# Kernel optimization log

Hardware: AMD Instinct MI355X
Metric: run time of the kernel (lower is better)

Reference implementation:

```python
import jax, jax.numpy as jnp
import numpy as np

TAIL_BOUND = 3.0
MIN_BIN_WIDTH = 1e-3
MIN_BIN_HEIGHT = 1e-3
SEARCH_EPS = 1e-6


def setup_inputs() -> dict:
    key = jax.random.key(0)
    k1, k2, k3, k4, k5 = jax.random.split(key, 5)
    B, D, K = 8192, 256, 8
    return {
        "x": jax.random.normal(k1, (B, D), dtype=jnp.float32),
        "w_": jax.random.normal(k2, (B, D, K), dtype=jnp.float32),
        "h_": jax.random.normal(k3, (B, D, K), dtype=jnp.float32),
        "dl_": jax.random.normal(k4, (B, D, 1), dtype=jnp.float32),
        "dr_": jax.random.normal(k5, (B, D, 1), dtype=jnp.float32),
    }


def _cumknots(unnorm, min_bin):
    # softmax -> min-width floor -> cumsum with exact 0/1 endpoints
    num_bins = unnorm.shape[-1]
    w = jax.nn.softmax(unnorm, axis=-1)
    w = min_bin + (1.0 - min_bin * num_bins) * w
    cum = jnp.cumsum(w, axis=-1)
    cum = cum.at[..., -1].set(1.0)
    pad = [(0, 0)] * (cum.ndim - 1) + [(1, 0)]
    cum = jnp.pad(cum, pad)
    return w, cum


def reference(x, w_, h_, dl_, dr_):
    num_bins = w_.shape[-1]
    left = bottom = -TAIL_BOUND
    right = top = TAIL_BOUND

    inside = (x >= left) & (x <= right)

    # map to unit interval; clamp keeps masked-out lanes numerically safe
    t = jnp.clip((x - left) / (right - left), 0.0, 1.0)

    widths, cumwidths = _cumknots(w_, MIN_BIN_WIDTH)       # [B,D,K], [B,D,K+1]
    heights, cumheights = _cumknots(h_, MIN_BIN_HEIGHT)

    slopes = heights / widths                              # [B,D,K]
    min1 = jnp.minimum(jnp.abs(slopes[..., :-1]), jnp.abs(slopes[..., 1:]))
    min2 = 0.5 * (widths[..., 1:] * slopes[..., :-1] + widths[..., :-1] * slopes[..., 1:]) \
           / (widths[..., :-1] + widths[..., 1:])
    mins = jnp.minimum(min1, min2)                         # [B,D,K-1]

    d_left = jax.nn.sigmoid(dl_) * 3.0 * slopes[..., :1]
    d_right = jax.nn.sigmoid(dr_) * 3.0 * slopes[..., -1:]
    d_mid = mins * (jnp.sign(slopes[..., :-1]) + jnp.sign(slopes[..., 1:]))
    derivs = jnp.concatenate([d_left, d_mid, d_right], axis=-1)  # [B,D,K+1]

    a = (derivs[..., :-1] + derivs[..., 1:] - 2.0 * slopes) / widths ** 2
    b = (3.0 * slopes - 2.0 * derivs[..., :-1] - derivs[..., 1:]) / widths
    c = derivs[..., :-1]
    d = cumheights[..., :-1]

    # searchsorted: sum(t >= knots) - 1, with eps bump on the last knot
    knots = cumwidths.at[..., -1].add(SEARCH_EPS)
    bin_idx = jnp.sum((t[..., None] >= knots).astype(jnp.int32), axis=-1) - 1
    bin_idx = jnp.clip(bin_idx, 0, num_bins - 1)[..., None]  # [B,D,1]

    take = lambda arr: jnp.take_along_axis(arr, bin_idx, axis=-1)[..., 0]
    ia, ib, ic, id_ = take(a), take(b), take(c), take(d)
    lw = take(cumwidths)

    sx = t - lw
    out_s = ia * sx ** 3 + ib * sx ** 2 + ic * sx + id_
    lad_s = jnp.log(jnp.abs(3.0 * ia * sx ** 2 + 2.0 * ib * sx + ic))

    out_s = jnp.clip(out_s, 0.0, 1.0) * (top - bottom) + bottom
    lad_s = lad_s + jnp.log(top - bottom) - jnp.log(right - left)

    outputs = jnp.where(inside, out_s, x)          # identity tails
    logabsdet = jnp.where(inside, lad_s, 0.0)
    return outputs, logabsdet
```

## Files before the change

kernel.cpp:

```cpp
#include <hip/hip_runtime.h>
#include <math.h>


constexpr int K = 8;
constexpr float TAIL = 3.0f;
constexpr float MIN_BIN = 0.001f;
constexpr float SEARCH_EPS = 1e-6f;

__device__ __forceinline__ float rcpf(float v) {
    return __builtin_amdgcn_rcpf(v);
}

__device__ __forceinline__ float signf(float v) {
    return (v > 0.0f ? 1.0f : (v < 0.0f ? -1.0f : 0.0f));
}

__global__ __launch_bounds__(256) void cbs_kernel(
    const float* __restrict__ x_,
    const float* __restrict__ w_,
    const float* __restrict__ h_,
    const float* __restrict__ dl_,
    const float* __restrict__ dr_,
    float* __restrict__ out,
    float* __restrict__ lad,
    int n)
{
    int i = blockIdx.x * blockDim.x + threadIdx.x;
    if (i >= n) return;

    const float4* w4 = (const float4*)w_ + 2 * (size_t)i;
    const float4* h4 = (const float4*)h_ + 2 * (size_t)i;
    float4 wa = w4[0], wb = w4[1];
    float4 ha = h4[0], hb = h4[1];

    float wr[K] = {wa.x, wa.y, wa.z, wa.w, wb.x, wb.y, wb.z, wb.w};
    float hr[K] = {ha.x, ha.y, ha.z, ha.w, hb.x, hb.y, hb.z, hb.w};

    float xv  = x_[i];
    float dlv = dl_[i];
    float drv = dr_[i];

    float mw = wr[0];
    #pragma unroll
    for (int k = 1; k < K; k++) mw = fmaxf(mw, wr[k]);
    float sw = 0.0f;
    #pragma unroll
    for (int k = 0; k < K; k++) { wr[k] = __expf(wr[k] - mw); sw += wr[k]; }
    float inv_sw = rcpf(sw);
    #pragma unroll
    for (int k = 0; k < K; k++) wr[k] = MIN_BIN + (1.0f - MIN_BIN * K) * (wr[k] * inv_sw);

    float mh = hr[0];
    #pragma unroll
    for (int k = 1; k < K; k++) mh = fmaxf(mh, hr[k]);
    float sh = 0.0f;
    #pragma unroll
    for (int k = 0; k < K; k++) { hr[k] = __expf(hr[k] - mh); sh += hr[k]; }
    float inv_sh = rcpf(sh);
    #pragma unroll
    for (int k = 0; k < K; k++) hr[k] = MIN_BIN + (1.0f - MIN_BIN * K) * (hr[k] * inv_sh);

    float cw[K + 1]; cw[0] = 0.0f;
    #pragma unroll
    for (int k = 0; k < K; k++) cw[k + 1] = cw[k] + wr[k];
    float ch[K + 1]; ch[0] = 0.0f;
    #pragma unroll
    for (int k = 0; k < K; k++) ch[k + 1] = ch[k] + hr[k];

    float s[K];
    #pragma unroll
    for (int k = 0; k < K; k++) s[k] = hr[k] * rcpf(wr[k]);

    float dv[K + 1];
    dv[0] = rcpf(1.0f + __expf(-dlv)) * 3.0f * s[0];
    dv[K] = rcpf(1.0f + __expf(-drv)) * 3.0f * s[K - 1];
    #pragma unroll
    for (int k = 0; k < K - 1; k++) {
        float m1 = fminf(fabsf(s[k]), fabsf(s[k + 1]));
        float m2 = 0.5f * (wr[k + 1] * s[k] + wr[k] * s[k + 1]) * rcpf(wr[k] + wr[k + 1]);
        float mn = fminf(m1, m2);
        dv[k + 1] = mn * (signf(s[k]) + signf(s[k + 1]));
    }

    float t = (xv + TAIL) * (1.0f / (2.0f * TAIL));
    t = fminf(fmaxf(t, 0.0f), 1.0f);

    int bin = 0;
    #pragma unroll
    for (int j = 1; j < K; j++) bin += (t >= cw[j]) ? 1 : 0;
    bin += (t >= 1.0f + SEARCH_EPS) ? 1 : 0;
    if (bin > K - 1) bin = K - 1;

    float wk = wr[0], sk = s[0], d0 = dv[0], d1 = dv[1], lw = cw[0], dd = ch[0];
    #pragma unroll
    for (int k = 1; k < K; k++) {
        bool sel = (bin == k);
        wk = sel ? wr[k]     : wk;
        sk = sel ? s[k]      : sk;
        d0 = sel ? dv[k]     : d0;
        d1 = sel ? dv[k + 1] : d1;
        lw = sel ? cw[k]     : lw;
        dd = sel ? ch[k]     : dd;
    }

    float inv_wk = rcpf(wk);
    float ia = (d0 + d1 - 2.0f * sk) * inv_wk * inv_wk;
    float ib = (3.0f * sk - 2.0f * d0 - d1) * inv_wk;
    float ic = d0;

    float sx = t - lw;
    float out_s = ((ia * sx + ib) * sx + ic) * sx + dd;
    float der   = (3.0f * ia * sx + 2.0f * ib) * sx + ic;
    float lad_s = __logf(fabsf(der));

    out_s = fminf(fmaxf(out_s, 0.0f), 1.0f) * (2.0f * TAIL) - TAIL;

    bool inside = (xv >= -TAIL) && (xv <= TAIL);
    out[i] = inside ? out_s : xv;
    lad[i] = inside ? lad_s : 0.0f;
}

extern "C" void kernel_launch(void* const* d_in, const int* in_sizes, int n_in,
                              void* d_out, int out_size, void* d_ws, size_t ws_size,
                              hipStream_t stream) {
    const float* x  = (const float*)d_in[0];
    const float* w  = (const float*)d_in[1];
    const float* h  = (const float*)d_in[2];
    const float* dl = (const float*)d_in[3];
    const float* dr = (const float*)d_in[4];
    int n = in_sizes[0];
    float* out = (float*)d_out;
    float* lad = out + n;

    const int threads = 256;
    const int blocks = (n + threads - 1) / threads;
    cbs_kernel<<<blocks, threads, 0, stream>>>(x, w, h, dl, dr, out, lad, n);
}
```

Baseline: 174.9 us.

## Process four elements per thread with vectorized IO and simplified spline math

Each thread now handles four consecutive elements, using float4 loads for x, dl and dr and float4 stores for both outputs. The softmax drops the max subtraction, the derivative formula is rewritten algebraically with fewer ops and no sign branches, and the bin search is folded into the predicated select loop. Launch bounds now request higher occupancy. The changes cut instruction count and memory transactions per element, but exp without the max shift can overflow for large logits, and the base>=n guard assumes n is a multiple of four.

New measurement: 179.0 us. +2.3%, slower.

```diff
diff --git a/kernel.cpp b/kernel.cpp
--- a/kernel.cpp
+++ b/kernel.cpp
@@ -3,19 +3,15 @@
 
 
 constexpr int K = 8;
+constexpr int E = 4;
 constexpr float TAIL = 3.0f;
 constexpr float MIN_BIN = 0.001f;
-constexpr float SEARCH_EPS = 1e-6f;
 
 __device__ __forceinline__ float rcpf(float v) {
     return __builtin_amdgcn_rcpf(v);
 }
 
-__device__ __forceinline__ float signf(float v) {
-    return (v > 0.0f ? 1.0f : (v < 0.0f ? -1.0f : 0.0f));
-}
-
-__global__ __launch_bounds__(256) void cbs_kernel(
+__global__ __launch_bounds__(256, 4) void cbs_kernel(
     const float* __restrict__ x_,
     const float* __restrict__ w_,
     const float* __restrict__ h_,
@@ -25,99 +21,102 @@
     float* __restrict__ lad,
     int n)
 {
-    int i = blockIdx.x * blockDim.x + threadIdx.x;
-    if (i >= n) return;
+    int tid  = blockIdx.x * blockDim.x + threadIdx.x;
+    int base = tid * E;
+    if (base >= n) return;
 
-    const float4* w4 = (const float4*)w_ + 2 * (size_t)i;
-    const float4* h4 = (const float4*)h_ + 2 * (size_t)i;
-    float4 wa = w4[0], wb = w4[1];
-    float4 ha = h4[0], hb = h4[1];
+    float4 xv4 = *(const float4*)(x_  + base);
+    float4 dl4 = *(const float4*)(dl_ + base);
+    float4 dr4 = *(const float4*)(dr_ + base);
+    const float4* w4 = (const float4*)w_ + 2 * (size_t)base;
+    const float4* h4 = (const float4*)h_ + 2 * (size_t)base;
 
-    float wr[K] = {wa.x, wa.y, wa.z, wa.w, wb.x, wb.y, wb.z, wb.w};
-    float hr[K] = {ha.x, ha.y, ha.z, ha.w, hb.x, hb.y, hb.z, hb.w};
-
-    float xv  = x_[i];
-    float dlv = dl_[i];
-    float drv = dr_[i];
-
-    float mw = wr[0];
+    float wv[E][K], hv[E][K];
     #pragma unroll
-    for (int k = 1; k < K; k++) mw = fmaxf(mw, wr[k]);
-    float sw = 0.0f;
+    for (int e = 0; e < E; e++) {
+        float4 a = w4[2 * e], b = w4[2 * e + 1];
+        wv[e][0] = a.x; wv[e][1] = a.y; wv[e][2] = a.z; wv[e][3] = a.w;
+        wv[e][4] = b.x; wv[e][5] = b.y; wv[e][6] = b.z; wv[e][7] = b.w;
+    }
     #pragma unroll
-    for (int k = 0; k < K; k++) { wr[k] = __expf(wr[k] - mw); sw += wr[k]; }
-    float inv_sw = rcpf(sw);
-    #pragma unroll
-    for (int k = 0; k < K; k++) wr[k] = MIN_BIN + (1.0f - MIN_BIN * K) * (wr[k] * inv_sw);
-
-    float mh = hr[0];
-    #pragma unroll
-    for (int k = 1; k < K; k++) mh = fmaxf(mh, hr[k]);
-    float sh = 0.0f;
-    #pragma unroll
-    for (int k = 0; k < K; k++) { hr[k] = __expf(hr[k] - mh); sh += hr[k]; }
-    float inv_sh = rcpf(sh);
-    #pragma unroll
-    for (int k = 0; k < K; k++) hr[k] = MIN_BIN + (1.0f - MIN_BIN * K) * (hr[k] * inv_sh);
-
-    float cw[K + 1]; cw[0] = 0.0f;
-    #pragma unroll
-    for (int k = 0; k < K; k++) cw[k + 1] = cw[k] + wr[k];
-    float ch[K + 1]; ch[0] = 0.0f;
-    #pragma unroll
-    for (int k = 0; k < K; k++) ch[k + 1] = ch[k] + hr[k];
-
-    float s[K];
-    #pragma unroll
-    for (int k = 0; k < K; k++) s[k] = hr[k] * rcpf(wr[k]);
-
-    float dv[K + 1];
-    dv[0] = rcpf(1.0f + __expf(-dlv)) * 3.0f * s[0];
-    dv[K] = rcpf(1.0f + __expf(-drv)) * 3.0f * s[K - 1];
-    #pragma unroll
-    for (int k = 0; k < K - 1; k++) {
-        float m1 = fminf(fabsf(s[k]), fabsf(s[k + 1]));
-        float m2 = 0.5f * (wr[k + 1] * s[k] + wr[k] * s[k + 1]) * rcpf(wr[k] + wr[k + 1]);
-        float mn = fminf(m1, m2);
-        dv[k + 1] = mn * (signf(s[k]) + signf(s[k + 1]));
+    for (int e = 0; e < E; e++) {
+        float4 a = h4[2 * e], b = h4[2 * e + 1];
+        hv[e][0] = a.x; hv[e][1] = a.y; hv[e][2] = a.z; hv[e][3] = a.w;
+        hv[e][4] = b.x; hv[e][5] = b.y; hv[e][6] = b.z; hv[e][7] = b.w;
     }
 
-    float t = (xv + TAIL) * (1.0f / (2.0f * TAIL));
-    t = fminf(fmaxf(t, 0.0f), 1.0f);
+    float xs[E]  = {xv4.x, xv4.y, xv4.z, xv4.w};
+    float dls[E] = {dl4.x, dl4.y, dl4.z, dl4.w};
+    float drs[E] = {dr4.x, dr4.y, dr4.z, dr4.w};
+    float outs[E], lads[E];
 
-    int bin = 0;
     #pragma unroll
-    for (int j = 1; j < K; j++) bin += (t >= cw[j]) ? 1 : 0;
-    bin += (t >= 1.0f + SEARCH_EPS) ? 1 : 0;
-    if (bin > K - 1) bin = K - 1;
+    for (int e = 0; e < E; e++) {
+        float wr[K], hr[K];
+        float sw = 0.0f, sh = 0.0f;
+        #pragma unroll
+        for (int k = 0; k < K; k++) { wr[k] = __expf(wv[e][k]); sw += wr[k]; }
+        #pragma unroll
+        for (int k = 0; k < K; k++) { hr[k] = __expf(hv[e][k]); sh += hr[k]; }
+        float cwf = (1.0f - MIN_BIN * K) * rcpf(sw);
+        float chf = (1.0f - MIN_BIN * K) * rcpf(sh);
+        #pragma unroll
+        for (int k = 0; k < K; k++) {
+            wr[k] = fmaf(wr[k], cwf, MIN_BIN);
+            hr[k] = fmaf(hr[k], chf, MIN_BIN);
+        }
 
-    float wk = wr[0], sk = s[0], d0 = dv[0], d1 = dv[1], lw = cw[0], dd = ch[0];
-    #pragma unroll
-    for (int k = 1; k < K; k++) {
-        bool sel = (bin == k);
-        wk = sel ? wr[k]     : wk;
-        sk = sel ? s[k]      : sk;
-        d0 = sel ? dv[k]     : d0;
-        d1 = sel ? dv[k + 1] : d1;
-        lw = sel ? cw[k]     : lw;
-        dd = sel ? ch[k]     : dd;
+        float cw[K + 1], ch[K + 1], s[K];
+        cw[0] = 0.0f; ch[0] = 0.0f;
+        #pragma unroll
+        for (int k = 0; k < K; k++) {
+            cw[k + 1] = cw[k] + wr[k];
+            ch[k + 1] = ch[k] + hr[k];
+            s[k] = hr[k] * rcpf(wr[k]);
+        }
+
+        float dv[K + 1];
+        dv[0] = 3.0f * s[0]     * rcpf(1.0f + __expf(-dls[e]));
+        dv[K] = 3.0f * s[K - 1] * rcpf(1.0f + __expf(-drs[e]));
+        #pragma unroll
+        for (int k = 0; k < K - 1; k++) {
+            float num = wr[k + 1] * s[k] + wr[k] * s[k + 1];
+            dv[k + 1] = fminf(2.0f * fminf(s[k], s[k + 1]),
+                              num * rcpf(wr[k] + wr[k + 1]));
+        }
+
+        float xv = xs[e];
+        float t = fminf(fmaxf((xv + TAIL) * (1.0f / (2.0f * TAIL)), 0.0f), 1.0f);
+
+        float wk = wr[0], sk = s[0], d0 = dv[0], d1 = dv[1], lw = 0.0f, dd = 0.0f;
+        #pragma unroll
+        for (int k = 1; k < K; k++) {
+            bool p = (t >= cw[k]);
+            wk = p ? wr[k]     : wk;
+            sk = p ? s[k]      : sk;
+            d0 = p ? dv[k]     : d0;
+            d1 = p ? dv[k + 1] : d1;
+            lw = p ? cw[k]     : lw;
+            dd = p ? ch[k]     : dd;
+        }
+
+        float iw = rcpf(wk);
+        float ia = (d0 + d1 - 2.0f * sk) * iw * iw;
+        float ib = (3.0f * sk - 2.0f * d0 - d1) * iw;
+        float sx = t - lw;
+        float out_s = ((ia * sx + ib) * sx + d0) * sx + dd;
+        float der   = (3.0f * ia * sx + 2.0f * ib) * sx + d0;
+        float lad_s = __logf(fabsf(der));
+
+        out_s = fminf(fmaxf(out_s, 0.0f), 1.0f) * (2.0f * TAIL) - TAIL;
+
+        bool inside = (xv >= -TAIL) && (xv <= TAIL);
+        outs[e] = inside ? out_s : xv;
+        lads[e] = inside ? lad_s : 0.0f;
     }
 
-    float inv_wk = rcpf(wk);
-    float ia = (d0 + d1 - 2.0f * sk) * inv_wk * inv_wk;
-    float ib = (3.0f * sk - 2.0f * d0 - d1) * inv_wk;
-    float ic = d0;
-
-    float sx = t - lw;
-    float out_s = ((ia * sx + ib) * sx + ic) * sx + dd;
-    float der   = (3.0f * ia * sx + 2.0f * ib) * sx + ic;
-    float lad_s = __logf(fabsf(der));
-
-    out_s = fminf(fmaxf(out_s, 0.0f), 1.0f) * (2.0f * TAIL) - TAIL;
-
-    bool inside = (xv >= -TAIL) && (xv <= TAIL);
-    out[i] = inside ? out_s : xv;
-    lad[i] = inside ? lad_s : 0.0f;
+    *(float4*)(out + base) = make_float4(outs[0], outs[1], outs[2], outs[3]);
+    *(float4*)(lad + base) = make_float4(lads[0], lads[1], lads[2], lads[3]);
 }
 
 extern "C" void kernel_launch(void* const* d_in, const int* in_sizes, int n_in,
@@ -133,6 +132,7 @@
     float* lad = out + n;
 
     const int threads = 256;
-    const int blocks = (n + threads - 1) / threads;
+    const int elems_per_block = threads * E;
+    const int blocks = (n + elems_per_block - 1) / elems_per_block;
     cbs_kernel<<<blocks, threads, 0, stream>>>(x, w, h, dl, dr, out, lad, n);
 }
```
